# Optimization experiments

Hardware: AMD Instinct MI355X
Metric: run time of the kernel (lower is better)

## Reference

```python
import jax, jax.numpy as jnp
import numpy as np

# static config (matches init_kwargs)
WS = (8, 7, 7)       # window size (T, H, W)
SS = (4, 3, 3)       # shift size (T, H, W)
NUM_HEADS = 4
B, T, H, W, C = 2, 16, 56, 56, 128
VOL = WS[0] * WS[1] * WS[2]  # 392 tokens per window


def _compute_attention_mask_3d(size_dhw, window_size, shift_size):
    """Static numpy replica of torch _compute_attention_mask_3d -> [nW, V, V]."""
    m = np.zeros(size_dhw, dtype=np.float32)
    slices = [((0, -window_size[i]), (-window_size[i], -shift_size[i]), (-shift_size[i], None))
              for i in range(3)]
    cnt = 0
    for d0, d1 in slices[0]:
        for h0, h1 in slices[1]:
            for w0, w1 in slices[2]:
                m[d0:d1, h0:h1, w0:w1] = cnt
                cnt += 1
    nT, nH, nW_ = (size_dhw[0] // window_size[0], size_dhw[1] // window_size[1],
                   size_dhw[2] // window_size[2])
    m = m.reshape(nT, window_size[0], nH, window_size[1], nW_, window_size[2])
    m = m.transpose(0, 2, 4, 1, 3, 5).reshape(nT * nH * nW_, VOL)
    diff = m[:, None, :] - m[:, :, None]
    return np.where(diff != 0, np.float32(-100.0), np.float32(0.0))


_ATTN_MASK = jnp.asarray(_compute_attention_mask_3d((T, H, W), WS, SS))  # [nW, V, V]


def setup_inputs() -> dict:
    key = jax.random.key(0)
    ks = jax.random.split(key, 6)
    s = 0.02
    return {
        "x": jax.random.normal(ks[0], (B, T, H, W, C), jnp.float32),
        "qkv_weight": jax.random.normal(ks[1], (3 * C, C), jnp.float32) * s,
        "qkv_bias": jax.random.normal(ks[2], (3 * C,), jnp.float32) * s,
        "proj_weight": jax.random.normal(ks[3], (C, C), jnp.float32) * s,
        "proj_bias": jax.random.normal(ks[4], (C,), jnp.float32) * s,
        "rel_pos_bias": jax.random.normal(ks[5], (1, NUM_HEADS, VOL, VOL), jnp.float32) * s,
    }


def reference(x, qkv_weight, qkv_bias, proj_weight, proj_bias, rel_pos_bias):
    b, t, h, w, c = x.shape
    hd = c // NUM_HEADS
    wt, wh, ww = WS
    nt, nh, nw = t // wt, h // wh, w // ww
    n_win = nt * nh * nw

    # cyclic shift (T,H,W divide the window so no padding needed)
    xs = jnp.roll(x, shift=(-SS[0], -SS[1], -SS[2]), axis=(1, 2, 3))

    # window partition -> [b*n_win, VOL, c]
    xw = xs.reshape(b, nt, wt, nh, wh, nw, ww, c)
    xw = xw.transpose(0, 1, 3, 5, 2, 4, 6, 7).reshape(b * n_win, VOL, c)

    # qkv projection
    qkv = xw @ qkv_weight.T + qkv_bias
    qkv = qkv.reshape(b * n_win, VOL, 3, NUM_HEADS, hd).transpose(2, 0, 3, 1, 4)
    q, k, v = qkv[0], qkv[1], qkv[2]          # [b*nW, nH, V, hd]
    q = q * (hd ** -0.5)

    attn = jnp.einsum("whqd,whkd->whqk", q, k) + rel_pos_bias
    # shift mask: broadcast over batch and heads
    attn = attn.reshape(b, n_win, NUM_HEADS, VOL, VOL) + _ATTN_MASK[None, :, None, :, :]
    attn = jax.nn.softmax(attn.reshape(b * n_win, NUM_HEADS, VOL, VOL), axis=-1)

    out = jnp.einsum("whqk,whkd->whqd", attn, v)         # [b*nW, nH, V, hd]
    out = out.transpose(0, 2, 1, 3).reshape(b * n_win, VOL, c)
    out = out @ proj_weight.T + proj_bias

    # window un-partition -> [b, t, h, w, c]
    out = out.reshape(b, nt, nh, nw, wt, wh, ww, c)
    out = out.transpose(0, 1, 4, 2, 5, 3, 6, 7).reshape(b, t, h, w, c)
    out = jnp.roll(out, shift=(SS[0], SS[1], SS[2]), axis=(1, 2, 3))
    return out
```

## Files before the change

### kernel.cpp

```cpp
#include <hip/hip_runtime.h>
#include <hip/hip_bf16.h>

typedef __bf16 bf16;
typedef __bf16 bf16x4 __attribute__((ext_vector_type(4)));
typedef __bf16 bf16x8 __attribute__((ext_vector_type(8)));
typedef float f32x4 __attribute__((ext_vector_type(4)));

#define MFMA(a, b, c) __builtin_amdgcn_mfma_f32_16x16x32_bf16(a, b, c, 0, 0, 0)

__device__ inline f32x4 zf4() { return f32x4{0.f, 0.f, 0.f, 0.f}; }

constexpr int Tc = 16, Hc = 56, Wc = 56, Cc = 128, NHc = 4, HDc = 32;
constexpr int VOL = 392;
constexpr int STc = 4, SHc = 3, SWc = 3;
constexpr int TWIN = 256;
constexpr int MTOT = TWIN * VOL;
constexpr int QSZ = TWIN * NHc * VOL * HDc;
constexpr int BMT_N = 4 * 400 * 416;
constexpr int OH_N = 8 * 416 * 32;

__device__ inline bf16x8 zero8() {
    bf16x8 z;
#pragma unroll
    for (int j = 0; j < 8; ++j) z[j] = (bf16)0.0f;
    return z;
}

__device__ inline f32x4 up4(bf16x4 b) {
    f32x4 r;
#pragma unroll
    for (int j = 0; j < 4; ++j) r[j] = (float)b[j];
    return r;
}

__device__ inline int cls_of(int v, int pt, int ph, int pw) {
    int tt = v / 49, rem = v % 49, hh = rem / 7, ww = rem % 7;
    int ct = pt ? (tt < 4 ? 1 : 2) : 0;
    int ch = ph ? (hh < 4 ? 1 : 2) : 0;
    int cw = pw ? (ww < 4 ? 1 : 2) : 0;
    return ct * 9 + ch * 3 + cw;
}

__global__ void cvt_params(const float* __restrict__ wq, const float* __restrict__ bq,
                           const float* __restrict__ wp, const float* __restrict__ bp,
                           bf16* __restrict__ wqb, bf16* __restrict__ bqb,
                           bf16* __restrict__ wpb, bf16* __restrict__ bpb) {
    int i = blockIdx.x * 256 + threadIdx.x;
    const float* s; bf16* d; int off;
    if (i < 12288)       { s = wq; d = wqb; off = i; }
    else if (i < 12384)  { s = bq; d = bqb; off = i - 12288; }
    else if (i < 16480)  { s = wp; d = wpb; off = i - 12384; }
    else if (i < 16512)  { s = bp; d = bpb; off = i - 16480; }
    else return;
    f32x4 v = *(const f32x4*)(s + (size_t)off * 4);
    bf16x4 o;
#pragma unroll
    for (int j = 0; j < 4; ++j) o[j] = (bf16)v[j];
    *(bf16x4*)(d + (size_t)off * 4) = o;
}

__global__ void biasprep_kernel(const float* __restrict__ rpb, bf16* __restrict__ bmt) {
    int i = blockIdx.x * 256 + threadIdx.x;
    if (i >= 4 * 400 * 104) return;
    int c4 = i % 104; int t = i / 104;
    int row = t % 400; int head = t / 400;
    f32x4 v;
    if (row >= VOL) {
#pragma unroll
        for (int j = 0; j < 4; ++j) v[j] = 0.f;
    } else if (c4 >= 98) {
#pragma unroll
        for (int j = 0; j < 4; ++j) v[j] = -144.0f;
    } else {
        f32x4 b = *(const f32x4*)(rpb + ((size_t)(head * VOL + row) * VOL + c4 * 4));
#pragma unroll
        for (int j = 0; j < 4; ++j) v[j] = b[j] * 1.4426950408889634f;
    }
    bf16x4 o;
#pragma unroll
    for (int j = 0; j < 4; ++j) o[j] = (bf16)v[j];
    *(bf16x4*)(bmt + ((size_t)(head * 400) * 416 + (size_t)(t % 400) * 416 - (size_t)(t % 400) * 416) + (size_t)t * 416 + c4 * 4) = o;
}

__global__ void ohprep_kernel(bf16* __restrict__ ohq, bf16* __restrict__ ohk) {
    int i = blockIdx.x * 256 + threadIdx.x;
    if (i >= 8 * 416) return;
    int tok = i % 416, pat = i / 416;
    int pt = (pat >> 2) & 1, ph = (pat >> 1) & 1, pw = pat & 1;
    int cls = (tok < VOL) ? cls_of(tok, pt, ph, pw) : -1;
    bf16* dq = ohq + (size_t)i * 32;
    bf16* dk = ohk + (size_t)i * 32;
    for (int ch = 0; ch < 32; ++ch) {
        float qv = (ch == cls) ? 12.0f : ((ch == 31) ? 12.0f : 0.f);
        float kv = (ch == cls) ? 12.0f : ((ch == 31) ? -12.0f : 0.f);
        dq[ch] = (bf16)qv;
        dk[ch] = (bf16)kv;
    }
}

__global__ __launch_bounds__(256, 2)
void qkv_kernel(const float* __restrict__ x, const bf16* __restrict__ wq,
                const bf16* __restrict__ bq, bf16* __restrict__ qws,
                bf16* __restrict__ kws, bf16* __restrict__ vws) {
    __shared__ bf16 As[64][136];
    __shared__ bf16 Cs[64][396];
    __shared__ unsigned int rb[64];
    __shared__ unsigned int rbw[64];
    const int tid = threadIdx.x;
    const int m0 = blockIdx.x * 64;

    if (tid < 64) {
        int g = m0 + tid;
        int win = g / VOL, tok = g % VOL;
        int b = win >> 7, wi = win & 127;
        int wt_i = wi >> 6, wh_i = (wi >> 3) & 7, ww_i = wi & 7;
        int tt = tok / 49, r2 = tok % 49, hh = r2 / 7, ww2 = r2 % 7;
        int t = wt_i * 8 + tt + STc; if (t >= Tc) t -= Tc;
        int h = wh_i * 7 + hh + SHc; if (h >= Hc) h -= Hc;
        int w = ww_i * 7 + ww2 + SWc; if (w >= Wc) w -= Wc;
        rb[tid] = (unsigned int)((((b * Tc + t) * Hc + h) * Wc + w) * Cc * 4);
        rbw[tid] = (unsigned int)((win << 9) | tok);
    }
    __syncthreads();

    for (int idx = tid; idx < 64 * 32; idx += 256) {
        int r = idx >> 5, c = idx & 31;
        const float* src = (const float*)((const char*)x + rb[r]) + c * 4;
        f32x4 v = *(const f32x4*)src;
        bf16x4 o;
#pragma unroll
        for (int j = 0; j < 4; ++j) o[j] = (bf16)v[j];
        *(bf16x4*)(&As[r][c * 4]) = o;
    }
    __syncthreads();

    const int wid = tid >> 6, lane = tid & 63;
    const int quad = lane >> 4, l15 = lane & 15;
    const int nbase = wid * 96;

    f32x4 acc[4][6];
#pragma unroll
    for (int ms = 0; ms < 4; ++ms)
#pragma unroll
        for (int nt = 0; nt < 6; ++nt) acc[ms][nt] = zf4();

#pragma unroll
    for (int ko = 0; ko < 4; ++ko) {
        bf16x8 af[4];
#pragma unroll
        for (int ms = 0; ms < 4; ++ms)
            af[ms] = *(const bf16x8*)(&As[ms * 16 + l15][ko * 32 + quad * 8]);
#pragma unroll
        for (int nt = 0; nt < 6; ++nt) {
            int n = nbase + nt * 16 + l15;
            bf16x8 bfrag = *(const bf16x8*)(wq + (size_t)n * Cc + ko * 32 + quad * 8);
#pragma unroll
            for (int ms = 0; ms < 4; ++ms)
                acc[ms][nt] = MFMA(af[ms], bfrag, acc[ms][nt]);
        }
    }

    float bcol[6];
#pragma unroll
    for (int nt = 0; nt < 6; ++nt) bcol[nt] = (float)bq[nbase + nt * 16 + l15];

#pragma unroll
    for (int nt = 0; nt < 6; ++nt) {
        int col = nbase + nt * 16 + l15;
        float scale = (col < 128) ? 0.25505653942f : 1.0f;
#pragma unroll
        for (int ms = 0; ms < 4; ++ms)
#pragma unroll
            for (int r = 0; r < 4; ++r) {
                int row = ms * 16 + quad * 4 + r;
                Cs[row][col] = (bf16)((acc[ms][nt][r] + bcol[nt]) * scale);
            }
    }
    __syncthreads();

    {
        int row = tid >> 2, hh4 = tid & 3;
        unsigned int p = rbw[row];
        int win = p >> 9, tok = p & 511;
        size_t off = ((size_t)(win * NHc + hh4) * VOL + tok) * HDc;
#pragma unroll
        for (int c = 0; c < 4; ++c) {
            bf16x4 lo = *(const bf16x4*)(&Cs[row][hh4 * 32 + c * 8]);
            bf16x4 hi = *(const bf16x4*)(&Cs[row][hh4 * 32 + c * 8 + 4]);
            *(bf16x8*)(qws + off + c * 8) = __builtin_shufflevector(lo, hi, 0, 1, 2, 3, 4, 5, 6, 7);
        }
#pragma unroll
        for (int c = 0; c < 4; ++c) {
            bf16x4 lo = *(const bf16x4*)(&Cs[row][128 + hh4 * 32 + c * 8]);
            bf16x4 hi = *(const bf16x4*)(&Cs[row][128 + hh4 * 32 + c * 8 + 4]);
            *(bf16x8*)(kws + off + c * 8) = __builtin_shufflevector(lo, hi, 0, 1, 2, 3, 4, 5, 6, 7);
        }
#pragma unroll
        for (int c = 0; c < 4; ++c) {
            bf16x4 lo = *(const bf16x4*)(&Cs[row][256 + hh4 * 32 + c * 8]);
            bf16x4 hi = *(const bf16x4*)(&Cs[row][256 + hh4 * 32 + c * 8 + 4]);
            *(bf16x8*)(vws + off + c * 8) = __builtin_shufflevector(lo, hi, 0, 1, 2, 3, 4, 5, 6, 7);
        }
    }
}

__global__ __launch_bounds__(512, 4)
void attn_kernel(const bf16* __restrict__ qws, const bf16* __restrict__ kws,
                 const bf16* __restrict__ vws, const bf16* __restrict__ bmt,
                 const bf16* __restrict__ ohqt, const bf16* __restrict__ ohkt,
                 bf16* __restrict__ aows) {
    __shared__ bf16 Kl[400][40];
    __shared__ bf16 Vt[32][424];
    __shared__ bf16 Pb[8][2][16][40];

    const int tid = threadIdx.x;
    const int win = blockIdx.x >> 2, head = blockIdx.x & 3;
    const int wi = win & 127;
    const int wt_i = wi >> 6, wh_i = (wi >> 3) & 7, ww_i = wi & 7;
    const int pat = ((wt_i == 1) << 2) | ((wh_i == 7) << 1) | (ww_i == 7);
    const bool masked = (pat != 0);

    const bf16* Qg = qws + (size_t)(win * NHc + head) * VOL * HDc;
    const bf16* Kg = kws + (size_t)(win * NHc + head) * VOL * HDc;
    const bf16* Vg = vws + (size_t)(win * NHc + head) * VOL * HDc;
    const bf16* Bg = bmt + (size_t)head * 400 * 416;
    const bf16* ohq_p = ohqt + (size_t)pat * 416 * 32;
    const bf16* ohk_p = ohkt + (size_t)pat * 416 * 32;

    for (int idx = tid; idx < 400 * 4; idx += 512) {
        int tok = idx >> 2, c = idx & 3;
        bf16x8 v = zero8();
        if (tok < VOL) v = *(const bf16x8*)(Kg + tok * HDc + c * 8);
        *(bf16x8*)(&Kl[tok][c * 8]) = v;
    }
    if (tid < 416) {
        int c = tid & 3, tok4 = (tid >> 2) * 4;
        bf16x8 rr[4];
#pragma unroll
        for (int i = 0; i < 4; ++i)
            rr[i] = (tok4 + i < VOL) ? *(const bf16x8*)(Vg + (tok4 + i) * HDc + c * 8) : zero8();
#pragma unroll
        for (int j = 0; j < 8; ++j) {
            bf16x4 wv;
            wv[0] = rr[0][j]; wv[1] = rr[1][j]; wv[2] = rr[2][j]; wv[3] = rr[3][j];
            *(bf16x4*)(&Vt[c * 8 + j][tok4]) = wv;
        }
    }
    __syncthreads();

    const int wid = tid >> 6, lane = tid & 63;
    const int quad = lane >> 4, l15 = lane & 15;
    bf16* PwA = &Pb[wid][0][0][0];
    bf16* PwB = &Pb[wid][1][0][0];

    for (int pass = 0; pass < 2; ++pass) {
        const int qtA = pass * 16 + wid, qtB = qtA + 8;
        const bool hasB = (qtB < 25);
        const int qbA = qtA * 16, qbB = qtB * 16;
        int qrA = qbA + l15; if (qrA >= VOL) qrA = VOL - 1;
        const bf16x8 qfA = *(const bf16x8*)(Qg + (size_t)qrA * HDc + quad * 8);
        const bf16* BrA = Bg + (size_t)(qbA + l15) * 416;
        const bf16* BrB = BrA;
        bf16x8 qfB, ohqA, ohqB;
        if (masked) ohqA = *(const bf16x8*)(ohq_p + (size_t)(qbA + l15) * 32 + quad * 8);
        if (hasB) {
            int qrB = qbB + l15; if (qrB >= VOL) qrB = VOL - 1;
            qfB = *(const bf16x8*)(Qg + (size_t)qrB * HDc + quad * 8);
            BrB = Bg + (size_t)(qbB + l15) * 416;
            if (masked) ohqB = *(const bf16x8*)(ohq_p + (size_t)(qbB + l15) * 32 + quad * 8);
        }
        f32x4 oA0 = zf4(), oA1 = zf4(), oB0 = zf4(), oB1 = zf4();
        float lsA = 0.f, lsB = 0.f;
        bf16x4 nbA0 = *(const bf16x4*)(BrA);
        bf16x4 nbA1 = *(const bf16x4*)(BrA + 16);
        bf16x4 nbB0, nbB1;
        if (hasB) { nbB0 = *(const bf16x4*)(BrB); nbB1 = *(const bf16x4*)(BrB + 16); }

        auto qk_full = [&](int kb) {
            bf16x8 kf0 = *(const bf16x8*)(&Kl[kb + l15][quad * 8]);
            bf16x8 kf1 = *(const bf16x8*)(&Kl[kb + 16 + l15][quad * 8]);
            bf16x8 ok0, ok1;
            if (masked) {
                ok0 = *(const bf16x8*)(ohk_p + (size_t)(kb + l15) * 32 + quad * 8);
                ok1 = *(const bf16x8*)(ohk_p + (size_t)(kb + 16 + l15) * 32 + quad * 8);
            }
            f32x4 cA0 = up4(nbA0), cA1 = up4(nbA1), cB0, cB1;
            if (hasB) { cB0 = up4(nbB0); cB1 = up4(nbB1); }
            if (kb < 384) {
                nbA0 = *(const bf16x4*)(BrA + kb + 32);
                nbA1 = *(const bf16x4*)(BrA + kb + 48);
                if (hasB) {
                    nbB0 = *(const bf16x4*)(BrB + kb + 32);
                    nbB1 = *(const bf16x4*)(BrB + kb + 48);
                }
            }
            if (masked) {
                cA0 = MFMA(ok0, ohqA, cA0);
                cA1 = MFMA(ok1, ohqA, cA1);
                if (hasB) { cB0 = MFMA(ok0, ohqB, cB0); cB1 = MFMA(ok1, ohqB, cB1); }
            }
            f32x4 sA0 = MFMA(kf0, qfA, cA0);
            f32x4 sA1 = MFMA(kf1, qfA, cA1);
            bf16x4 pA0, pA1;
            float la = 0.f;
#pragma unroll
            for (int r = 0; r < 4; ++r) {
                float e0 = __builtin_amdgcn_exp2f(sA0[r]);
                float e1 = __builtin_amdgcn_exp2f(sA1[r]);
                pA0[r] = (bf16)e0; pA1[r] = (bf16)e1; la += e0 + e1;
            }
            lsA += la;
            *(bf16x4*)(PwA + l15 * 40 + quad * 4) = pA0;
            *(bf16x4*)(PwA + l15 * 40 + 16 + quad * 4) = pA1;
            if (hasB) {
                f32x4 sB0 = MFMA(kf0, qfB, cB0);
                f32x4 sB1 = MFMA(kf1, qfB, cB1);
                bf16x4 pB0, pB1;
                float lb = 0.f;
#pragma unroll
                for (int r = 0; r < 4; ++r) {
                    float e0 = __builtin_amdgcn_exp2f(sB0[r]);
                    float e1 = __builtin_amdgcn_exp2f(sB1[r]);
                    pB0[r] = (bf16)e0; pB1[r] = (bf16)e1; lb += e0 + e1;
                }
                lsB += lb;
                *(bf16x4*)(PwB + l15 * 40 + quad * 4) = pB0;
                *(bf16x4*)(PwB + l15 * 40 + 16 + quad * 4) = pB1;
            }
        };
        auto pv = [&](int kb) {
            bf16x8 pfA = *(const bf16x8*)(PwA + l15 * 40 + quad * 8);
            bf16x8 pfB;
            if (hasB) pfB = *(const bf16x8*)(PwB + l15 * 40 + quad * 8);
            bf16x8 vf0 = *(const bf16x8*)(&Vt[l15][kb + quad * 8]);
            bf16x8 vf1 = *(const bf16x8*)(&Vt[16 + l15][kb + quad * 8]);
            oA0 = MFMA(vf0, pfA, oA0);
            oA1 = MFMA(vf1, pfA, oA1);
            if (hasB) { oB0 = MFMA(vf0, pfB, oB0); oB1 = MFMA(vf1, pfB, oB1); }
        };

        qk_full(0);
#pragma unroll 1
        for (int kt = 1; kt < 12; ++kt) {
            pv((kt - 1) * 32);
            qk_full(kt * 32);
        }
        pv(352);
        {
            bf16x8 kf0 = *(const bf16x8*)(&Kl[384 + l15][quad * 8]);
            bf16x8 ok0;
            if (masked) ok0 = *(const bf16x8*)(ohk_p + (size_t)(384 + l15) * 32 + quad * 8);
            f32x4 cA0 = up4(nbA0), cB0;
            if (hasB) cB0 = up4(nbB0);
            if (masked) {
                cA0 = MFMA(ok0, ohqA, cA0);
                if (hasB) cB0 = MFMA(ok0, ohqB, cB0);
            }
            f32x4 sA0 = MFMA(kf0, qfA, cA0);
            bf16x4 pA0, z4;
            float la = 0.f;
#pragma unroll
            for (int r = 0; r < 4; ++r) {
                float e0 = __builtin_amdgcn_exp2f(sA0[r]);
                pA0[r] = (bf16)e0; la += e0; z4[r] = (bf16)0.f;
            }
            lsA += la;
            *(bf16x4*)(PwA + l15 * 40 + quad * 4) = pA0;
            *(bf16x4*)(PwA + l15 * 40 + 16 + quad * 4) = z4;
            if (hasB) {
                f32x4 sB0 = MFMA(kf0, qfB, cB0);
                bf16x4 pB0;
                float lb = 0.f;
#pragma unroll
                for (int r = 0; r < 4; ++r) {
                    float e0 = __builtin_amdgcn_exp2f(sB0[r]);
                    pB0[r] = (bf16)e0; lb += e0;
                }
                lsB += lb;
                *(bf16x4*)(PwB + l15 * 40 + quad * 4) = pB0;
                *(bf16x4*)(PwB + l15 * 40 + 16 + quad * 4) = z4;
            }
        }
        pv(384);

        lsA += __shfl_xor(lsA, 16); lsA += __shfl_xor(lsA, 32);
        if (hasB) { lsB += __shfl_xor(lsB, 16); lsB += __shfl_xor(lsB, 32); }
        if (qbA + l15 < VOL) {
            float inv = 1.f / lsA;
            bf16x4 w0, w1;
#pragma unroll
            for (int r = 0; r < 4; ++r) { w0[r] = (bf16)(oA0[r] * inv); w1[r] = (bf16)(oA1[r] * inv); }
            bf16* dst = aows + ((size_t)win * VOL + qbA + l15) * Cc + head * HDc;
            *(bf16x4*)(dst + quad * 4) = w0;
            *(bf16x4*)(dst + 16 + quad * 4) = w1;
        }
        if (hasB && qbB + l15 < VOL) {
            float inv = 1.f / lsB;
            bf16x4 w0, w1;
#pragma unroll
            for (int r = 0; r < 4; ++r) { w0[r] = (bf16)(oB0[r] * inv); w1[r] = (bf16)(oB1[r] * inv); }
            bf16* dst = aows + ((size_t)win * VOL + qbB + l15) * Cc + head * HDc;
            *(bf16x4*)(dst + quad * 4) = w0;
            *(bf16x4*)(dst + 16 + quad * 4) = w1;
        }
    }
}

__global__ __launch_bounds__(256, 2)
void proj_kernel(const bf16* __restrict__ aows, const bf16* __restrict__ wp,
                 const bf16* __restrict__ bp, float* __restrict__ out) {
    __shared__ bf16 As[64][136];
    __shared__ float Csf[64][132];
    __shared__ unsigned int rbo[64];
    const int tid = threadIdx.x;
    const int m0 = blockIdx.x * 64;

    if (tid < 64) {
        int g = m0 + tid;
        int win = g / VOL, tok = g % VOL;
        int b = win >> 7, wi = win & 127;
        int wt_i = wi >> 6, wh_i = (wi >> 3) & 7, ww_i = wi & 7;
        int tt = tok / 49, r2 = tok % 49, hh = r2 / 7, ww2 = r2 % 7;
        int t = wt_i * 8 + tt + STc; if (t >= Tc) t -= Tc;
        int h = wh_i * 7 + hh + SHc; if (h >= Hc) h -= Hc;
        int w = ww_i * 7 + ww2 + SWc; if (w >= Wc) w -= Wc;
        rbo[tid] = (unsigned int)((((b * Tc + t) * Hc + h) * Wc + w) * Cc * 4);
    }
    for (int idx = tid; idx < 64 * 16; idx += 256) {
        int r = idx >> 4, c = idx & 15;
        *(bf16x8*)(&As[r][c * 8]) = *(const bf16x8*)(aows + (size_t)(m0 + r) * Cc + c * 8);
    }
    __syncthreads();

    const int wid = tid >> 6, lane = tid & 63;
    const int quad = lane >> 4, l15 = lane & 15;

    f32x4 acc[8];
#pragma unroll
    for (int nt = 0; nt < 8; ++nt) acc[nt] = zf4();

#pragma unroll
    for (int ko = 0; ko < 4; ++ko) {
        bf16x8 af = *(const bf16x8*)(&As[wid * 16 + l15][ko * 32 + quad * 8]);
#pragma unroll
        for (int nt = 0; nt < 8; ++nt) {
            bf16x8 bfrag = *(const bf16x8*)(wp + (size_t)(nt * 16 + l15) * Cc + ko * 32 + quad * 8);
            acc[nt] = MFMA(af, bfrag, acc[nt]);
        }
    }
#pragma unroll
    for (int nt = 0; nt < 8; ++nt) {
        float bv = (float)bp[nt * 16 + l15];
#pragma unroll
        for (int r = 0; r < 4; ++r) {
            int row = wid * 16 + quad * 4 + r;
            Csf[row][nt * 16 + l15] = acc[nt][r] + bv;
        }
    }
    __syncthreads();

    for (int idx = tid; idx < 64 * 32; idx += 256) {
        int row = idx >> 5, ch = idx & 31;
        float* dst = (float*)((char*)out + rbo[row]) + ch * 4;
        *(f32x4*)dst = *(const f32x4*)(&Csf[row][ch * 4]);
    }
}

extern "C" void kernel_launch(void* const* d_in, const int* in_sizes, int n_in,
                              void* d_out, int out_size, void* d_ws, size_t ws_size,
                              hipStream_t stream) {
    const float* x    = (const float*)d_in[0];
    const float* wqf  = (const float*)d_in[1];
    const float* bqf  = (const float*)d_in[2];
    const float* wpf  = (const float*)d_in[3];
    const float* bpf  = (const float*)d_in[4];
    const float* rpbf = (const float*)d_in[5];
    float* out = (float*)d_out;

    bf16* wqb  = (bf16*)d_ws;
    bf16* bqb  = wqb + 49152;
    bf16* wpb  = bqb + 384;
    bf16* bpb  = wpb + 16384;
    bf16* bmt  = bpb + 128;
    bf16* ohq  = bmt + BMT_N;
    bf16* ohk  = ohq + OH_N;
    bf16* qws  = ohk + OH_N;
    bf16* kws  = qws + QSZ;
    bf16* vws  = kws + QSZ;
    bf16* aows = vws + QSZ;

    hipLaunchKernelGGL(cvt_params, dim3(65), dim3(256), 0, stream,
                       wqf, bqf, wpf, bpf, wqb, bqb, wpb, bpb);
    hipLaunchKernelGGL(biasprep_kernel, dim3((4 * 400 * 104 + 255) / 256), dim3(256), 0, stream,
                       rpbf, bmt);
    hipLaunchKernelGGL(ohprep_kernel, dim3((8 * 416 + 255) / 256), dim3(256), 0, stream,
                       ohq, ohk);
    hipLaunchKernelGGL(qkv_kernel, dim3(MTOT / 64), dim3(256), 0, stream,
                       x, wqb, bqb, qws, kws, vws);
    hipLaunchKernelGGL(attn_kernel, dim3(TWIN * NHc), dim3(512), 0, stream,
                       qws, kws, vws, bmt, ohq, ohk, aows);
    hipLaunchKernelGGL(proj_kernel, dim3(MTOT / 64), dim3(256), 0, stream,
                       aows, wpb, bpb, out);
}
```

Baseline: 273.2 us.

## Fold shift mask into per-pattern bias tables and transpose GEMM operand roles

Precomputes one combined relative-position-bias plus shift-mask table for each of the 8 boundary patterns. This removes the one-hot MFMA mask trick and its extra global loads from the attention inner loop. The three prep kernels are merged into one launch. The QKV and projection GEMMs swap operand order so each lane writes contiguous 4-element vectors to shared memory, and the attention bias reads are adjusted to match. The cost is a bias table eight times larger, which puts more pressure on L2.

```diff
diff --git a/kernel.cpp b/kernel.cpp
--- a/kernel.cpp
+++ b/kernel.cpp
@@ -16,8 +16,7 @@
 constexpr int TWIN = 256;
 constexpr int MTOT = TWIN * VOL;
 constexpr int QSZ = TWIN * NHc * VOL * HDc;
-constexpr int BMT_N = 4 * 400 * 416;
-constexpr int OH_N = 8 * 416 * 32;
+constexpr int BMT_N = 8 * 4 * 400 * 416;
 
 __device__ inline bf16x8 zero8() {
     bf16x8 z;
@@ -41,60 +40,59 @@
     return ct * 9 + ch * 3 + cw;
 }
 
-__global__ void cvt_params(const float* __restrict__ wq, const float* __restrict__ bq,
-                           const float* __restrict__ wp, const float* __restrict__ bp,
-                           bf16* __restrict__ wqb, bf16* __restrict__ bqb,
-                           bf16* __restrict__ wpb, bf16* __restrict__ bpb) {
-    int i = blockIdx.x * 256 + threadIdx.x;
-    const float* s; bf16* d; int off;
-    if (i < 12288)       { s = wq; d = wqb; off = i; }
-    else if (i < 12384)  { s = bq; d = bqb; off = i - 12288; }
-    else if (i < 16480)  { s = wp; d = wpb; off = i - 12384; }
-    else if (i < 16512)  { s = bp; d = bpb; off = i - 16480; }
-    else return;
-    f32x4 v = *(const f32x4*)(s + (size_t)off * 4);
-    bf16x4 o;
-#pragma unroll
-    for (int j = 0; j < 4; ++j) o[j] = (bf16)v[j];
-    *(bf16x4*)(d + (size_t)off * 4) = o;
-}
-
-__global__ void biasprep_kernel(const float* __restrict__ rpb, bf16* __restrict__ bmt) {
-    int i = blockIdx.x * 256 + threadIdx.x;
-    if (i >= 4 * 400 * 104) return;
-    int c4 = i % 104; int t = i / 104;
-    int row = t % 400; int head = t / 400;
-    f32x4 v;
-    if (row >= VOL) {
-#pragma unroll
-        for (int j = 0; j < 4; ++j) v[j] = 0.f;
-    } else if (c4 >= 98) {
-#pragma unroll
-        for (int j = 0; j < 4; ++j) v[j] = -144.0f;
-    } else {
-        f32x4 b = *(const f32x4*)(rpb + ((size_t)(head * VOL + row) * VOL + c4 * 4));
-#pragma unroll
-        for (int j = 0; j < 4; ++j) v[j] = b[j] * 1.4426950408889634f;
-    }
-    bf16x4 o;
-#pragma unroll
-    for (int j = 0; j < 4; ++j) o[j] = (bf16)v[j];
-    *(bf16x4*)(bmt + ((size_t)(head * 400) * 416 + (size_t)(t % 400) * 416 - (size_t)(t % 400) * 416) + (size_t)t * 416 + c4 * 4) = o;
-}
-
-__global__ void ohprep_kernel(bf16* __restrict__ ohq, bf16* __restrict__ ohk) {
-    int i = blockIdx.x * 256 + threadIdx.x;
-    if (i >= 8 * 416) return;
-    int tok = i % 416, pat = i / 416;
+__global__ void prep_kernel(const float* __restrict__ wq, const float* __restrict__ bq,
+                            const float* __restrict__ wp, const float* __restrict__ bp,
+                            const float* __restrict__ rpb,
+                            bf16* __restrict__ wqb, bf16* __restrict__ bqb,
+                            bf16* __restrict__ wpb, bf16* __restrict__ bpb,
+                            bf16* __restrict__ bmt) {
+    const int blk = blockIdx.x, tid = threadIdx.x;
+    if (blk < 65) {
+        int i = blk * 256 + tid;
+        const float* s; bf16* d; int off;
+        if (i < 12288)       { s = wq; d = wqb; off = i; }
+        else if (i < 12384)  { s = bq; d = bqb; off = i - 12288; }
+        else if (i < 16480)  { s = wp; d = wpb; off = i - 12384; }
+        else if (i < 16512)  { s = bp; d = bpb; off = i - 16480; }
+        else return;
+        f32x4 v = *(const f32x4*)(s + (size_t)off * 4);
+        bf16x4 o;
+#pragma unroll
+        for (int j = 0; j < 4; ++j) o[j] = (bf16)v[j];
+        *(bf16x4*)(d + (size_t)off * 4) = o;
+        return;
+    }
+    __shared__ unsigned char clsc[392];
+    int bb = blk - 65;
+    int pat = bb / 100, rem = bb % 100;
+    int head = rem / 25, rc = rem % 25;
     int pt = (pat >> 2) & 1, ph = (pat >> 1) & 1, pw = pat & 1;
-    int cls = (tok < VOL) ? cls_of(tok, pt, ph, pw) : -1;
-    bf16* dq = ohq + (size_t)i * 32;
-    bf16* dk = ohk + (size_t)i * 32;
-    for (int ch = 0; ch < 32; ++ch) {
-        float qv = (ch == cls) ? 12.0f : ((ch == 31) ? 12.0f : 0.f);
-        float kv = (ch == cls) ? 12.0f : ((ch == 31) ? -12.0f : 0.f);
-        dq[ch] = (bf16)qv;
-        dk[ch] = (bf16)kv;
+    for (int v = tid; v < 392; v += 256) clsc[v] = (unsigned char)cls_of(v, pt, ph, pw);
+    __syncthreads();
+    bf16* dst = bmt + ((size_t)(pat * NHc + head) * 400 + rc * 16) * 416;
+    for (int idx = tid; idx < 16 * 104; idx += 256) {
+        int lr = idx / 104, c4 = idx % 104;
+        int row = rc * 16 + lr;
+        bf16x4 o;
+        if (row >= VOL) {
+#pragma unroll
+            for (int j = 0; j < 4; ++j) o[j] = (bf16)0.f;
+        } else {
+            int rcls = clsc[row];
+            const float* brow = rpb + (size_t)(head * VOL + row) * VOL;
+#pragma unroll
+            for (int j = 0; j < 4; ++j) {
+                int col = c4 * 4 + j;
+                float v;
+                if (col >= VOL) v = -144.0f;
+                else {
+                    v = brow[col] * 1.4426950408889634f;
+                    if (clsc[col] != rcls) v -= 144.0f;
+                }
+                o[j] = (bf16)v;
+            }
+        }
+        *(bf16x4*)(dst + (size_t)lr * 416 + c4 * 4) = o;
     }
 }
 
@@ -138,43 +136,40 @@
     const int quad = lane >> 4, l15 = lane & 15;
     const int nbase = wid * 96;
 
-    f32x4 acc[4][6];
-#pragma unroll
-    for (int ms = 0; ms < 4; ++ms)
-#pragma unroll
-        for (int nt = 0; nt < 6; ++nt) acc[ms][nt] = zf4();
+    f32x4 acc[6][4];
+#pragma unroll
+    for (int mt = 0; mt < 6; ++mt)
+#pragma unroll
+        for (int nt = 0; nt < 4; ++nt) acc[mt][nt] = zf4();
 
 #pragma unroll
     for (int ko = 0; ko < 4; ++ko) {
-        bf16x8 af[4];
-#pragma unroll
-        for (int ms = 0; ms < 4; ++ms)
-            af[ms] = *(const bf16x8*)(&As[ms * 16 + l15][ko * 32 + quad * 8]);
-#pragma unroll
-        for (int nt = 0; nt < 6; ++nt) {
-            int n = nbase + nt * 16 + l15;
-            bf16x8 bfrag = *(const bf16x8*)(wq + (size_t)n * Cc + ko * 32 + quad * 8);
-#pragma unroll
-            for (int ms = 0; ms < 4; ++ms)
-                acc[ms][nt] = MFMA(af[ms], bfrag, acc[ms][nt]);
-        }
-    }
-
-    float bcol[6];
-#pragma unroll
-    for (int nt = 0; nt < 6; ++nt) bcol[nt] = (float)bq[nbase + nt * 16 + l15];
-
-#pragma unroll
-    for (int nt = 0; nt < 6; ++nt) {
-        int col = nbase + nt * 16 + l15;
-        float scale = (col < 128) ? 0.25505653942f : 1.0f;
-#pragma unroll
-        for (int ms = 0; ms < 4; ++ms)
-#pragma unroll
-            for (int r = 0; r < 4; ++r) {
-                int row = ms * 16 + quad * 4 + r;
-                Cs[row][col] = (bf16)((acc[ms][nt][r] + bcol[nt]) * scale);
-            }
+        bf16x8 xf[4];
+#pragma unroll
+        for (int nt = 0; nt < 4; ++nt)
+            xf[nt] = *(const bf16x8*)(&As[nt * 16 + l15][ko * 32 + quad * 8]);
+#pragma unroll
+        for (int mt = 0; mt < 6; ++mt) {
+            bf16x8 wf = *(const bf16x8*)(wq + (size_t)(nbase + mt * 16 + l15) * Cc + ko * 32 + quad * 8);
+#pragma unroll
+            for (int nt = 0; nt < 4; ++nt)
+                acc[mt][nt] = MFMA(wf, xf[nt], acc[mt][nt]);
+        }
+    }
+
+#pragma unroll
+    for (int mt = 0; mt < 6; ++mt) {
+        int colbase = nbase + mt * 16 + quad * 4;
+        bf16x4 bc = *(const bf16x4*)(bq + colbase);
+        float scale = (colbase < 128) ? 0.25505653942f : 1.0f;
+#pragma unroll
+        for (int nt = 0; nt < 4; ++nt) {
+            bf16x4 o;
+#pragma unroll
+            for (int r = 0; r < 4; ++r)
+                o[r] = (bf16)((acc[mt][nt][r] + (float)bc[r]) * scale);
+            *(bf16x4*)(&Cs[nt * 16 + l15][colbase]) = o;
+        }
     }
     __syncthreads();
 
@@ -207,7 +202,6 @@
 __global__ __launch_bounds__(512, 4)
 void attn_kernel(const bf16* __restrict__ qws, const bf16* __restrict__ kws,
                  const bf16* __restrict__ vws, const bf16* __restrict__ bmt,
-                 const bf16* __restrict__ ohqt, const bf16* __restrict__ ohkt,
                  bf16* __restrict__ aows) {
     __shared__ bf16 Kl[400][40];
     __shared__ bf16 Vt[32][424];
@@ -218,14 +212,11 @@
     const int wi = win & 127;
     const int wt_i = wi >> 6, wh_i = (wi >> 3) & 7, ww_i = wi & 7;
     const int pat = ((wt_i == 1) << 2) | ((wh_i == 7) << 1) | (ww_i == 7);
-    const bool masked = (pat != 0);
 
     const bf16* Qg = qws + (size_t)(win * NHc + head) * VOL * HDc;
     const bf16* Kg = kws + (size_t)(win * NHc + head) * VOL * HDc;
     const bf16* Vg = vws + (size_t)(win * NHc + head) * VOL * HDc;
-    const bf16* Bg = bmt + (size_t)head * 400 * 416;
-    const bf16* ohq_p = ohqt + (size_t)pat * 416 * 32;
-    const bf16* ohk_p = ohkt + (size_t)pat * 416 * 32;
+    const bf16* Bg = bmt + (size_t)(pat * NHc + head) * 400 * 416;
 
     for (int idx = tid; idx < 400 * 4; idx += 512) {
         int tok = idx >> 2, c = idx & 3;
@@ -261,43 +252,34 @@
         const bf16x8 qfA = *(const bf16x8*)(Qg + (size_t)qrA * HDc + quad * 8);
         const bf16* BrA = Bg + (size_t)(qbA + l15) * 416;
         const bf16* BrB = BrA;
-        bf16x8 qfB, ohqA, ohqB;
-        if (masked) ohqA = *(const bf16x8*)(ohq_p + (size_t)(qbA + l15) * 32 + quad * 8);
+        bf16x8 qfB;
         if (hasB) {
             int qrB = qbB + l15; if (qrB >= VOL) qrB = VOL - 1;
             qfB = *(const bf16x8*)(Qg + (size_t)qrB * HDc + quad * 8);
             BrB = Bg + (size_t)(qbB + l15) * 416;
-            if (masked) ohqB = *(const bf16x8*)(ohq_p + (size_t)(qbB + l15) * 32 + quad * 8);
         }
         f32x4 oA0 = zf4(), oA1 = zf4(), oB0 = zf4(), oB1 = zf4();
         float lsA = 0.f, lsB = 0.f;
-        bf16x4 nbA0 = *(const bf16x4*)(BrA);
-        bf16x4 nbA1 = *(const bf16x4*)(BrA + 16);
+        bf16x4 nbA0 = *(const bf16x4*)(BrA + quad * 4);
+        bf16x4 nbA1 = *(const bf16x4*)(BrA + 16 + quad * 4);
         bf16x4 nbB0, nbB1;
-        if (hasB) { nbB0 = *(const bf16x4*)(BrB); nbB1 = *(const bf16x4*)(BrB + 16); }
+        if (hasB) {
+            nbB0 = *(const bf16x4*)(BrB + quad * 4);
+            nbB1 = *(const bf16x4*)(BrB + 16 + quad * 4);
+        }
 
         auto qk_full = [&](int kb) {
             bf16x8 kf0 = *(const bf16x8*)(&Kl[kb + l15][quad * 8]);
             bf16x8 kf1 = *(const bf16x8*)(&Kl[kb + 16 + l15][quad * 8]);
-            bf16x8 ok0, ok1;
-            if (masked) {
-                ok0 = *(const bf16x8*)(ohk_p + (size_t)(kb + l15) * 32 + quad * 8);
-                ok1 = *(const bf16x8*)(ohk_p + (size_t)(kb + 16 + l15) * 32 + quad * 8);
-            }
             f32x4 cA0 = up4(nbA0), cA1 = up4(nbA1), cB0, cB1;
             if (hasB) { cB0 = up4(nbB0); cB1 = up4(nbB1); }
             if (kb < 384) {
-                nbA0 = *(const bf16x4*)(BrA + kb + 32);
-                nbA1 = *(const bf16x4*)(BrA + kb + 48);
+                nbA0 = *(const bf16x4*)(BrA + kb + 32 + quad * 4);
+                nbA1 = *(const bf16x4*)(BrA + kb + 48 + quad * 4);
                 if (hasB) {
-                    nbB0 = *(const bf16x4*)(BrB + kb + 32);
-                    nbB1 = *(const bf16x4*)(BrB + kb + 48);
+                    nbB0 = *(const bf16x4*)(BrB + kb + 32 + quad * 4);
+                    nbB1 = *(const bf16x4*)(BrB + kb + 48 + quad * 4);
                 }
-            }
-            if (masked) {
-                cA0 = MFMA(ok0, ohqA, cA0);
-                cA1 = MFMA(ok1, ohqA, cA1);
-                if (hasB) { cB0 = MFMA(ok0, ohqB, cB0); cB1 = MFMA(ok1, ohqB, cB1); }
             }
             f32x4 sA0 = MFMA(kf0, qfA, cA0);
             f32x4 sA1 = MFMA(kf1, qfA, cA1);
@@ -348,14 +330,8 @@
         pv(352);
         {
             bf16x8 kf0 = *(const bf16x8*)(&Kl[384 + l15][quad * 8]);
-            bf16x8 ok0;
-            if (masked) ok0 = *(const bf16x8*)(ohk_p + (size_t)(384 + l15) * 32 + quad * 8);
             f32x4 cA0 = up4(nbA0), cB0;
             if (hasB) cB0 = up4(nbB0);
-            if (masked) {
-                cA0 = MFMA(ok0, ohqA, cA0);
-                if (hasB) cB0 = MFMA(ok0, ohqB, cB0);
-            }
             f32x4 sA0 = MFMA(kf0, qfA, cA0);
             bf16x4 pA0, z4;
             float la = 0.f;
@@ -437,25 +413,25 @@
 
     f32x4 acc[8];
 #pragma unroll
-    for (int nt = 0; nt < 8; ++nt) acc[nt] = zf4();
+    for (int mt = 0; mt < 8; ++mt) acc[mt] = zf4();
 
 #pragma unroll
     for (int ko = 0; ko < 4; ++ko) {
-        bf16x8 af = *(const bf16x8*)(&As[wid * 16 + l15][ko * 32 + quad * 8]);
-#pragma unroll
-        for (int nt = 0; nt < 8; ++nt) {
-            bf16x8 bfrag = *(const bf16x8*)(wp + (size_t)(nt * 16 + l15) * Cc + ko * 32 + quad * 8);
-            acc[nt] = MFMA(af, bfrag, acc[nt]);
-        }
-    }
-#pragma unroll
-    for (int nt = 0; nt < 8; ++nt) {
-        float bv = (float)bp[nt * 16 + l15];
-#pragma unroll
-        for (int r = 0; r < 4; ++r) {
-            int row = wid * 16 + quad * 4 + r;
-            Csf[row][nt * 16 + l15] = acc[nt][r] + bv;
-        }
+        bf16x8 xf = *(const bf16x8*)(&As[wid * 16 + l15][ko * 32 + quad * 8]);
+#pragma unroll
+        for (int mt = 0; mt < 8; ++mt) {
+            bf16x8 wf = *(const bf16x8*)(wp + (size_t)(mt * 16 + l15) * Cc + ko * 32 + quad * 8);
+            acc[mt] = MFMA(wf, xf, acc[mt]);
+        }
+    }
+#pragma unroll
+    for (int mt = 0; mt < 8; ++mt) {
+        int colbase = mt * 16 + quad * 4;
+        bf16x4 bc = *(const bf16x4*)(bp + colbase);
+        f32x4 o;
+#pragma unroll
+        for (int r = 0; r < 4; ++r) o[r] = acc[mt][r] + (float)bc[r];
+        *(f32x4*)(&Csf[wid * 16 + l15][colbase]) = o;
     }
     __syncthreads();
 
@@ -482,23 +458,17 @@
     bf16* wpb  = bqb + 384;
     bf16* bpb  = wpb + 16384;
     bf16* bmt  = bpb + 128;
-    bf16* ohq  = bmt + BMT_N;
-    bf16* ohk  = ohq + OH_N;
-    bf16* qws  = ohk + OH_N;
+    bf16* qws  = bmt + BMT_N;
     bf16* kws  = qws + QSZ;
     bf16* vws  = kws + QSZ;
     bf16* aows = vws + QSZ;
 
-    hipLaunchKernelGGL(cvt_params, dim3(65), dim3(256), 0, stream,
-                       wqf, bqf, wpf, bpf, wqb, bqb, wpb, bpb);
-    hipLaunchKernelGGL(biasprep_kernel, dim3((4 * 400 * 104 + 255) / 256), dim3(256), 0, stream,
-                       rpbf, bmt);
-    hipLaunchKernelGGL(ohprep_kernel, dim3((8 * 416 + 255) / 256), dim3(256), 0, stream,
-                       ohq, ohk);
+    hipLaunchKernelGGL(prep_kernel, dim3(865), dim3(256), 0, stream,
+                       wqf, bqf, wpf, bpf, rpbf, wqb, bqb, wpb, bpb, bmt);
     hipLaunchKernelGGL(qkv_kernel, dim3(MTOT / 64), dim3(256), 0, stream,
                        x, wqb, bqb, qws, kws, vws);
     hipLaunchKernelGGL(attn_kernel, dim3(TWIN * NHc), dim3(512), 0, stream,
-                       qws, kws, vws, bmt, ohq, ohk, aows);
+                       qws, kws, vws, bmt, aows);
     hipLaunchKernelGGL(proj_kernel, dim3(MTOT / 64), dim3(256), 0, stream,
                        aows, wpb, bpb, out);
 }
```

New measurement: 255.7 us. 1.07x faster.
